# Performance work log

Hardware: AMD Instinct MI355X
Metric: run time of the kernel (lower is better)

## Reference

```python
import jax, jax.numpy as jnp
import numpy as np

B, H, S, D = 4, 16, 2048, 64

def setup_inputs() -> dict:
    key = jax.random.key(0)
    kq, kk, kv, km = jax.random.split(key, 4)
    Q = jax.random.normal(kq, (B, H, S, D), dtype=jnp.float32)
    K = jax.random.normal(kk, (B, H, S, D), dtype=jnp.float32)
    V = jax.random.normal(kv, (B, H, S, D), dtype=jnp.float32)
    mask = jax.random.randint(km, (B, 1, 1, S), 0, 2, dtype=jnp.int32)
    return {"Q": Q, "K": K, "V": V, "mask": mask}

def reference(Q, K, V, mask):
    d_k = Q.shape[-1]
    scaling = jax.lax.rsqrt(jnp.asarray(d_k, dtype=Q.dtype))
    # [B,H,S,S] attention scores
    scores = jnp.einsum("bhqd,bhkd->bhqk", Q, K) * scaling
    scores = jnp.where(mask == 1, jnp.asarray(-jnp.inf, dtype=scores.dtype), scores)
    attn_weights = jax.nn.softmax(scores, axis=-1)
    output = jnp.einsum("bhqk,bhkd->bhqd", attn_weights, V)
    return output, attn_weights
```

## Files before the change

### kernel.cpp

```cpp
#include <hip/hip_runtime.h>
#include <hip/hip_bf16.h>

#define B_ 4
#define H_ 16
#define S_ 2048
#define D_ 64

#define KS 72
#define PS 72

typedef __attribute__((ext_vector_type(8))) short bf16x8;
typedef __attribute__((ext_vector_type(4))) float f32x4;

__device__ __forceinline__ short f2bf(float x) {
    __hip_bfloat16 h = __float2bfloat16(x);
    union { __hip_bfloat16 h; short s; } u;
    u.h = h;
    return u.s;
}

__global__ __launch_bounds__(256, 2)
void attn_kernel(const float* __restrict__ Q, const float* __restrict__ K,
                 const float* __restrict__ V, const int* __restrict__ mask,
                 float* __restrict__ out, float* __restrict__ wout)
{
    __shared__ __align__(16) short Ksh[64 * KS];
    __shared__ __align__(16) short Vsh[64 * KS];
    __shared__ __align__(16) short Psh[4][16 * PS];
    __shared__ int msh[64];

    const int tid  = threadIdx.x;
    const int wave = tid >> 6;
    const int lane = tid & 63;
    const int quad = lane >> 4;
    const int col  = lane & 15;

    const int bh = blockIdx.x >> 5;
    const int qt = blockIdx.x & 31;
    const int q0 = qt * 64 + wave * 16;

    const float* Qh = Q + (size_t)bh * S_ * D_;
    const float* Kh = K + (size_t)bh * S_ * D_;
    const float* Vh = V + (size_t)bh * S_ * D_;
    const int*   mk = mask + (size_t)(bh >> 4) * S_;
    float* outh = out  + (size_t)bh * S_ * D_;
    float* wh   = wout + (size_t)bh * S_ * S_;

    bf16x8 qf[2];
    {
        const float* qp = Qh + (size_t)(q0 + col) * D_ + quad * 8;
        #pragma unroll
        for (int c = 0; c < 2; ++c) {
            bf16x8 v;
            #pragma unroll
            for (int j = 0; j < 8; ++j) v[j] = f2bf(qp[c * 32 + j]);
            qf[c] = v;
        }
    }

    const int srow = tid >> 2;
    const int sd0  = (tid & 3) * 16;

    float rsum[4] = {0.f, 0.f, 0.f, 0.f};
    for (int kt = 0; kt < S_; kt += 64) {
        __syncthreads();
        {
            const float4* kp4 = (const float4*)(Kh + (size_t)(kt + srow) * D_ + sd0);
            float4 a = kp4[0], b = kp4[1], c = kp4[2], d = kp4[3];
            bf16x8 lo, hi;
            lo[0]=f2bf(a.x); lo[1]=f2bf(a.y); lo[2]=f2bf(a.z); lo[3]=f2bf(a.w);
            lo[4]=f2bf(b.x); lo[5]=f2bf(b.y); lo[6]=f2bf(b.z); lo[7]=f2bf(b.w);
            hi[0]=f2bf(c.x); hi[1]=f2bf(c.y); hi[2]=f2bf(c.z); hi[3]=f2bf(c.w);
            hi[4]=f2bf(d.x); hi[5]=f2bf(d.y); hi[6]=f2bf(d.z); hi[7]=f2bf(d.w);
            *(bf16x8*)&Ksh[srow * KS + sd0]     = lo;
            *(bf16x8*)&Ksh[srow * KS + sd0 + 8] = hi;
            if (tid < 64) msh[tid] = mk[kt + tid];
        }
        __syncthreads();
        #pragma unroll
        for (int sub = 0; sub < 4; ++sub) {
            const short* kb = &Ksh[(sub * 16 + col) * KS + quad * 8];
            bf16x8 kf0 = *(const bf16x8*)kb;
            bf16x8 kf1 = *(const bf16x8*)(kb + 32);
            f32x4 acc = {0.f, 0.f, 0.f, 0.f};
            acc = __builtin_amdgcn_mfma_f32_16x16x32_bf16(qf[0], kf0, acc, 0, 0, 0);
            acc = __builtin_amdgcn_mfma_f32_16x16x32_bf16(qf[1], kf1, acc, 0, 0, 0);
            const int mv = msh[sub * 16 + col];
            #pragma unroll
            for (int i = 0; i < 4; ++i) {
                float p = (mv == 1) ? 0.f : __expf(acc[i] * 0.125f);
                rsum[i] += p;
            }
        }
    }
    #pragma unroll
    for (int off = 1; off < 16; off <<= 1) {
        #pragma unroll
        for (int i = 0; i < 4; ++i) rsum[i] += __shfl_xor(rsum[i], off);
    }
    float rinv[4];
    #pragma unroll
    for (int i = 0; i < 4; ++i) rinv[i] = 1.0f / rsum[i];

    f32x4 oacc[4];
    #pragma unroll
    for (int nt = 0; nt < 4; ++nt) oacc[nt] = (f32x4){0.f, 0.f, 0.f, 0.f};

    short* pw = Psh[wave];
    for (int kt = 0; kt < S_; kt += 64) {
        __syncthreads();
        {
            const float4* kp4 = (const float4*)(Kh + (size_t)(kt + srow) * D_ + sd0);
            float4 a = kp4[0], b = kp4[1], c = kp4[2], d = kp4[3];
            bf16x8 lo, hi;
            lo[0]=f2bf(a.x); lo[1]=f2bf(a.y); lo[2]=f2bf(a.z); lo[3]=f2bf(a.w);
            lo[4]=f2bf(b.x); lo[5]=f2bf(b.y); lo[6]=f2bf(b.z); lo[7]=f2bf(b.w);
            hi[0]=f2bf(c.x); hi[1]=f2bf(c.y); hi[2]=f2bf(c.z); hi[3]=f2bf(c.w);
            hi[4]=f2bf(d.x); hi[5]=f2bf(d.y); hi[6]=f2bf(d.z); hi[7]=f2bf(d.w);
            *(bf16x8*)&Ksh[srow * KS + sd0]     = lo;
            *(bf16x8*)&Ksh[srow * KS + sd0 + 8] = hi;

            const float4* vp4 = (const float4*)(Vh + (size_t)(kt + srow) * D_ + sd0);
            float4 va = vp4[0], vb = vp4[1], vc = vp4[2], vd = vp4[3];
            float vv[16] = {va.x, va.y, va.z, va.w, vb.x, vb.y, vb.z, vb.w,
                            vc.x, vc.y, vc.z, vc.w, vd.x, vd.y, vd.z, vd.w};
            #pragma unroll
            for (int j = 0; j < 16; ++j)
                Vsh[(sd0 + j) * KS + srow] = f2bf(vv[j]);

            if (tid < 64) msh[tid] = mk[kt + tid];
        }
        __syncthreads();
        #pragma unroll
        for (int sub = 0; sub < 4; ++sub) {
            const short* kb = &Ksh[(sub * 16 + col) * KS + quad * 8];
            bf16x8 kf0 = *(const bf16x8*)kb;
            bf16x8 kf1 = *(const bf16x8*)(kb + 32);
            f32x4 acc = {0.f, 0.f, 0.f, 0.f};
            acc = __builtin_amdgcn_mfma_f32_16x16x32_bf16(qf[0], kf0, acc, 0, 0, 0);
            acc = __builtin_amdgcn_mfma_f32_16x16x32_bf16(qf[1], kf1, acc, 0, 0, 0);
            const int mv = msh[sub * 16 + col];
            #pragma unroll
            for (int i = 0; i < 4; ++i) {
                float p = (mv == 1) ? 0.f : __expf(acc[i] * 0.125f) * rinv[i];
                wh[(size_t)(q0 + quad * 4 + i) * S_ + kt + sub * 16 + col] = p;
                pw[(quad * 4 + i) * PS + sub * 16 + col] = f2bf(p);
            }
        }
        __syncthreads();
        #pragma unroll
        for (int c = 0; c < 2; ++c) {
            bf16x8 af = *(const bf16x8*)&pw[col * PS + c * 32 + quad * 8];
            #pragma unroll
            for (int nt = 0; nt < 4; ++nt) {
                bf16x8 vf = *(const bf16x8*)&Vsh[(nt * 16 + col) * KS + c * 32 + quad * 8];
                oacc[nt] = __builtin_amdgcn_mfma_f32_16x16x32_bf16(af, vf, oacc[nt], 0, 0, 0);
            }
        }
    }

    #pragma unroll
    for (int nt = 0; nt < 4; ++nt) {
        #pragma unroll
        for (int i = 0; i < 4; ++i)
            outh[(size_t)(q0 + quad * 4 + i) * D_ + nt * 16 + col] = oacc[nt][i];
    }
}

extern "C" void kernel_launch(void* const* d_in, const int* in_sizes, int n_in,
                              void* d_out, int out_size, void* d_ws, size_t ws_size,
                              hipStream_t stream) {
    const float* Q    = (const float*)d_in[0];
    const float* K    = (const float*)d_in[1];
    const float* V    = (const float*)d_in[2];
    const int*   mask = (const int*)d_in[3];
    float* out  = (float*)d_out;
    float* wout = out + (size_t)B_ * H_ * S_ * D_;

    dim3 grid(B_ * H_ * S_ / 64);
    attn_kernel<<<grid, 256, 0, stream>>>(Q, K, V, mask, out, wout);
}
```

Measured before the change: 1.444 ms.

## Precast K/V to swizzled bf16 scratch and stream tiles via direct LDS loads

Adds a prep kernel that converts K and V to bf16 once per head, storing XOR-swizzled tiles (V transposed) in workspace. The attention kernel then copies tiles straight into LDS with global_load_lds instead of having every query block reload fp32 K/V and convert it, and it raises the occupancy hint to 4. Probabilities are staged as fp32 in LDS so the attention-weight writes become coalesced float4 stores. This costs an extra kernel launch and a scratch round trip, and it only takes effect when the workspace is large enough.

```diff
diff --git a/kernel.cpp b/kernel.cpp
--- a/kernel.cpp
+++ b/kernel.cpp
@@ -6,6 +6,11 @@
 #define S_ 2048
 #define D_ 64
 
+#define NTILE (S_ / 64)
+#define TILE_SH (64 * 64)
+#define HEAD_SH (NTILE * TILE_SH)
+#define NHEAD (B_ * H_)
+
 #define KS 72
 #define PS 72
 
@@ -13,10 +18,192 @@
 typedef __attribute__((ext_vector_type(4))) float f32x4;
 
 __device__ __forceinline__ short f2bf(float x) {
-    __hip_bfloat16 h = __float2bfloat16(x);
     union { __hip_bfloat16 h; short s; } u;
-    u.h = h;
+    u.h = __float2bfloat16(x);
     return u.s;
+}
+
+typedef const __attribute__((address_space(1))) void GVp;
+typedef __attribute__((address_space(3))) void LVp;
+
+__device__ __forceinline__ void gll16(const void* g, void* l) {
+    __builtin_amdgcn_global_load_lds((GVp*)g, (LVp*)l, 16, 0, 0);
+}
+
+__global__ __launch_bounds__(256)
+void prep_kernel(const float* __restrict__ K, const float* __restrict__ V,
+                 short* __restrict__ kscr, short* __restrict__ vscr)
+{
+    const int gid = blockIdx.x * 256 + threadIdx.x;
+    const int NK = NHEAD * S_ * (D_ / 8);
+    if (gid < NK) {
+        const int dc  = gid & 7;
+        const int key = (gid >> 3) & (S_ - 1);
+        const int bh  = gid >> 14;
+        const float* src = K + ((size_t)bh * S_ + key) * D_ + dc * 8;
+        bf16x8 v;
+        #pragma unroll
+        for (int j = 0; j < 8; ++j) v[j] = f2bf(src[j]);
+        const int kt = key >> 6, row = key & 63;
+        short* dst = kscr + (size_t)bh * HEAD_SH + (size_t)kt * TILE_SH
+                   + row * 64 + ((dc * 8) ^ ((row & 7) * 8));
+        *(bf16x8*)dst = v;
+    } else {
+        const int g  = gid - NK;
+        const int d  = g & 63;
+        const int kc = (g >> 6) & 7;
+        const int kt = (g >> 9) & 31;
+        const int bh = g >> 14;
+        const float* src = V + ((size_t)bh * S_ + kt * 64 + kc * 8) * D_ + d;
+        bf16x8 v;
+        #pragma unroll
+        for (int j = 0; j < 8; ++j) v[j] = f2bf(src[j * D_]);
+        short* dst = vscr + (size_t)bh * HEAD_SH + (size_t)kt * TILE_SH
+                   + d * 64 + ((kc * 8) ^ ((d & 7) * 8));
+        *(bf16x8*)dst = v;
+    }
+}
+
+__global__ __launch_bounds__(256, 4)
+void attn2_kernel(const float* __restrict__ Q, const int* __restrict__ mask,
+                  const short* __restrict__ kscr, const short* __restrict__ vscr,
+                  float* __restrict__ out, float* __restrict__ wout)
+{
+    __shared__ __align__(16) short Ksh[TILE_SH];
+    __shared__ __align__(16) short Vsh[TILE_SH];
+    __shared__ __align__(16) float Pf[4][16 * 68];
+    __shared__ int msh[64];
+
+    const int tid  = threadIdx.x;
+    const int wave = tid >> 6;
+    const int lane = tid & 63;
+    const int quad = lane >> 4;
+    const int col  = lane & 15;
+
+    const int bh = blockIdx.x >> 5;
+    const int qt = blockIdx.x & 31;
+    const int q0 = qt * 64 + wave * 16;
+
+    const float* Qh = Q + (size_t)bh * S_ * D_;
+    const int*   mk = mask + (size_t)(bh >> 4) * S_;
+    const short* kb_head = kscr + (size_t)bh * HEAD_SH;
+    const short* vb_head = vscr + (size_t)bh * HEAD_SH;
+    float* outh = out  + (size_t)bh * S_ * D_;
+    float* wh   = wout + (size_t)bh * S_ * S_;
+
+    bf16x8 qf[2];
+    {
+        const float4* qp4 = (const float4*)(Qh + (size_t)(q0 + col) * D_ + quad * 8);
+        float4 a = qp4[0], b = qp4[1], c = qp4[8], d = qp4[9];
+        bf16x8 t0, t1;
+        t0[0]=f2bf(a.x); t0[1]=f2bf(a.y); t0[2]=f2bf(a.z); t0[3]=f2bf(a.w);
+        t0[4]=f2bf(b.x); t0[5]=f2bf(b.y); t0[6]=f2bf(b.z); t0[7]=f2bf(b.w);
+        t1[0]=f2bf(c.x); t1[1]=f2bf(c.y); t1[2]=f2bf(c.z); t1[3]=f2bf(c.w);
+        t1[4]=f2bf(d.x); t1[5]=f2bf(d.y); t1[6]=f2bf(d.z); t1[7]=f2bf(d.w);
+        qf[0] = t0; qf[1] = t1;
+    }
+
+    float rsum[4] = {0.f, 0.f, 0.f, 0.f};
+    for (int tt = 0; tt < NTILE; ++tt) {
+        __syncthreads();
+        const short* ks = kb_head + (size_t)tt * TILE_SH;
+        gll16(ks + tid * 8,        &Ksh[wave * 512]);
+        gll16(ks + 2048 + tid * 8, &Ksh[2048 + wave * 512]);
+        if (tid < 64) msh[tid] = mk[tt * 64 + tid];
+        __syncthreads();
+        #pragma unroll
+        for (int sub = 0; sub < 4; ++sub) {
+            const int row = sub * 16 + col;
+            const short* kb = &Ksh[row * 64];
+            const int sw = (row & 7) * 8;
+            bf16x8 kf0 = *(const bf16x8*)&kb[(quad * 8) ^ sw];
+            bf16x8 kf1 = *(const bf16x8*)&kb[(quad * 8 + 32) ^ sw];
+            f32x4 acc = {0.f, 0.f, 0.f, 0.f};
+            acc = __builtin_amdgcn_mfma_f32_16x16x32_bf16(qf[0], kf0, acc, 0, 0, 0);
+            acc = __builtin_amdgcn_mfma_f32_16x16x32_bf16(qf[1], kf1, acc, 0, 0, 0);
+            const int mv = msh[row];
+            #pragma unroll
+            for (int i = 0; i < 4; ++i) {
+                float p = (mv == 1) ? 0.f : __expf(acc[i] * 0.125f);
+                rsum[i] += p;
+            }
+        }
+    }
+    #pragma unroll
+    for (int off = 1; off < 16; off <<= 1) {
+        #pragma unroll
+        for (int i = 0; i < 4; ++i) rsum[i] += __shfl_xor(rsum[i], off);
+    }
+    float rinv[4];
+    #pragma unroll
+    for (int i = 0; i < 4; ++i) rinv[i] = 1.0f / rsum[i];
+
+    f32x4 oacc[4];
+    #pragma unroll
+    for (int nt = 0; nt < 4; ++nt) oacc[nt] = (f32x4){0.f, 0.f, 0.f, 0.f};
+
+    float* pw = Pf[wave];
+    for (int tt = 0; tt < NTILE; ++tt) {
+        __syncthreads();
+        const short* ks = kb_head + (size_t)tt * TILE_SH;
+        const short* vs = vb_head + (size_t)tt * TILE_SH;
+        gll16(ks + tid * 8,        &Ksh[wave * 512]);
+        gll16(ks + 2048 + tid * 8, &Ksh[2048 + wave * 512]);
+        gll16(vs + tid * 8,        &Vsh[wave * 512]);
+        gll16(vs + 2048 + tid * 8, &Vsh[2048 + wave * 512]);
+        if (tid < 64) msh[tid] = mk[tt * 64 + tid];
+        __syncthreads();
+
+        #pragma unroll
+        for (int sub = 0; sub < 4; ++sub) {
+            const int row = sub * 16 + col;
+            const short* kb = &Ksh[row * 64];
+            const int sw = (row & 7) * 8;
+            bf16x8 kf0 = *(const bf16x8*)&kb[(quad * 8) ^ sw];
+            bf16x8 kf1 = *(const bf16x8*)&kb[(quad * 8 + 32) ^ sw];
+            f32x4 acc = {0.f, 0.f, 0.f, 0.f};
+            acc = __builtin_amdgcn_mfma_f32_16x16x32_bf16(qf[0], kf0, acc, 0, 0, 0);
+            acc = __builtin_amdgcn_mfma_f32_16x16x32_bf16(qf[1], kf1, acc, 0, 0, 0);
+            const int mv = msh[row];
+            #pragma unroll
+            for (int i = 0; i < 4; ++i) {
+                float p = (mv == 1) ? 0.f : __expf(acc[i] * 0.125f) * rinv[i];
+                pw[(quad * 4 + i) * 68 + row] = p;
+            }
+        }
+        __syncthreads();
+
+        #pragma unroll
+        for (int it = 0; it < 4; ++it) {
+            const int r = it * 4 + quad;
+            f32x4 pv = *(const f32x4*)&pw[r * 68 + col * 4];
+            *(f32x4*)&wh[(size_t)(q0 + r) * S_ + tt * 64 + col * 4] = pv;
+        }
+
+        #pragma unroll
+        for (int c = 0; c < 2; ++c) {
+            const float* pr = &pw[col * 68 + c * 32 + quad * 8];
+            f32x4 p0 = *(const f32x4*)pr;
+            f32x4 p1 = *(const f32x4*)(pr + 4);
+            bf16x8 af;
+            af[0]=f2bf(p0[0]); af[1]=f2bf(p0[1]); af[2]=f2bf(p0[2]); af[3]=f2bf(p0[3]);
+            af[4]=f2bf(p1[0]); af[5]=f2bf(p1[1]); af[6]=f2bf(p1[2]); af[7]=f2bf(p1[3]);
+            const int ko = c * 32 + quad * 8;
+            #pragma unroll
+            for (int nt = 0; nt < 4; ++nt) {
+                const int dr = nt * 16 + col;
+                bf16x8 vf = *(const bf16x8*)&Vsh[dr * 64 + (ko ^ ((dr & 7) * 8))];
+                oacc[nt] = __builtin_amdgcn_mfma_f32_16x16x32_bf16(af, vf, oacc[nt], 0, 0, 0);
+            }
+        }
+    }
+
+    #pragma unroll
+    for (int nt = 0; nt < 4; ++nt) {
+        #pragma unroll
+        for (int i = 0; i < 4; ++i)
+            outh[(size_t)(q0 + quad * 4 + i) * D_ + nt * 16 + col] = oacc[nt][i];
+    }
 }
 
 __global__ __launch_bounds__(256, 2)
@@ -177,6 +364,14 @@
     float* out  = (float*)d_out;
     float* wout = out + (size_t)B_ * H_ * S_ * D_;
 
-    dim3 grid(B_ * H_ * S_ / 64);
-    attn_kernel<<<grid, 256, 0, stream>>>(Q, K, V, mask, out, wout);
-}
+    const size_t scratch_need = (size_t)2 * NHEAD * HEAD_SH * sizeof(short);
+    if (d_ws && ws_size >= scratch_need) {
+        short* kscr = (short*)d_ws;
+        short* vscr = kscr + (size_t)NHEAD * HEAD_SH;
+        const int nchunks = 2 * NHEAD * S_ * (D_ / 8);
+        prep_kernel<<<nchunks / 256, 256, 0, stream>>>(K, V, kscr, vscr);
+        attn2_kernel<<<B_ * H_ * S_ / 64, 256, 0, stream>>>(Q, mask, kscr, vscr, out, wout);
+    } else {
+        attn_kernel<<<B_ * H_ * S_ / 64, 256, 0, stream>>>(Q, K, V, mask, out, wout);
+    }
+}
```

Measured after the change: 1.318 ms. 8.7% less time.
